# Performance work log

Measured on AMD Instinct MI355X. Metric: run time of the kernel, lower is better.

The kernel has to match this reference:

```python
import jax, jax.numpy as jnp
import numpy as np

N, E = 50000, 1600000
IN, OUT, H = 128, 32, 2
NT, ET = 20, 4
ETE, EAE, ED = 16, 16, 16
SLOPE = 0.2  # conv_neg_slope


def setup_inputs() -> dict:
    key = jax.random.key(0)
    ks = jax.random.split(key, 11)
    d_att = 2 * OUT + ETE + EAE
    return dict(
        x=jax.random.normal(ks[0], (N, IN), jnp.float32),
        edge_index=jax.random.randint(ks[1], (2, E), 0, N),
        ntypes=jax.random.randint(ks[2], (N,), 0, NT),
        etypes=jax.random.randint(ks[3], (E,), 0, ET),
        eattr=jax.random.normal(ks[4], (E, ED), jnp.float32),
        het_W=jax.random.normal(ks[5], (NT, IN, OUT), jnp.float32) / np.sqrt(IN).astype(np.float32),
        het_b=jnp.zeros((NT, OUT), jnp.float32),
        etype_table=jax.random.normal(ks[6], (ET, ETE), jnp.float32),
        eattr_W=jax.random.normal(ks[7], (ED, EAE), jnp.float32) / np.sqrt(ED).astype(np.float32),
        att_W=jax.random.normal(ks[8], (d_att, H), jnp.float32) / np.sqrt(d_att).astype(np.float32),
        lin_W=jax.random.normal(ks[9], (OUT + EAE, OUT), jnp.float32) / np.sqrt(OUT + EAE).astype(np.float32),
    )


def _lrelu(v):
    return jax.nn.leaky_relu(v, SLOPE)


def _heat_conv(x, edge_index, ntypes, etypes, eattr,
               het_W, het_b, etype_table, eattr_W, att_W, lin_W):
    # HeteroLinear: node-type-conditioned linear transform (loop over 20 types,
    # avoids materializing a [N, IN, OUT] gathered-weight tensor)
    h = jnp.zeros((x.shape[0], het_W.shape[-1]), x.dtype)
    for t in range(het_W.shape[0]):
        h = h + jnp.where((ntypes == t)[:, None], x @ het_W[t] + het_b[t], 0.0)

    src, dst = edge_index[0], edge_index[1]
    ete = _lrelu(etype_table[etypes])        # [E, ETE] edge-type embedding
    ea = _lrelu(eattr @ eattr_W)             # [E, EAE] edge-attr embedding
    x_i = h[dst]                             # target node feats [E, OUT]
    x_j = h[src]                             # source node feats [E, OUT]

    feat = jnp.concatenate([x_i, x_j, ete, ea], axis=-1)
    alpha = _lrelu(feat @ att_W)             # [E, H] raw attention logits

    # softmax grouped by destination node, per head
    amax = jax.ops.segment_max(alpha, dst, num_segments=N)  # [N, H]
    alpha = jnp.exp(alpha - amax[dst])
    denom = jax.ops.segment_sum(alpha, dst, num_segments=N)  # [N, H]
    alpha = alpha / denom[dst]

    msg = jnp.concatenate([x_j, ea], axis=-1) @ lin_W        # [E, OUT]
    m = (msg[:, None, :] * alpha[:, :, None]).reshape(alpha.shape[0], H * OUT)
    out = jax.ops.segment_sum(m, dst, num_segments=N)        # [N, H*OUT]
    return out  # concat=True -> flattened heads


def reference(x, edge_index, ntypes, etypes, eattr,
              het_W, het_b, etype_table, eattr_W, att_W, lin_W):
    out = _heat_conv(x, edge_index, ntypes, etypes, eattr,
                     het_W, het_b, etype_table, eattr_W, att_W, lin_W)
    return jax.nn.relu(out)  # final activation in forward (eval mode: no dropout)
```

## Files before the change

kernel.cpp:

```cpp
#include <hip/hip_runtime.h>
#include <hip/hip_fp16.h>

#define NN 50000
#define EE 1600000
#define IN_F 128
#define OUT_F 32
#define NHEAD 2
#define ETE_F 16
#define EAE_F 16
#define ED_F 16
#define D_ATT 96
#define SLOPE 0.2f
#define NB_SCAN 196

__global__ __launch_bounds__(256) void k_hetlin(
    const float* __restrict__ x, const int* __restrict__ ntypes,
    const float* __restrict__ hetW, const float* __restrict__ hetb,
    float* __restrict__ h)
{
    int tid = blockIdx.x * 256 + threadIdx.x;
    int n = tid >> 5;
    int o = tid & 31;
    if (n >= NN) return;
    int t = ntypes[n];
    const float* W = hetW + (size_t)t * IN_F * OUT_F + o;
    const float* xr = x + (size_t)n * IN_F;
    float acc = hetb[t * OUT_F + o];
    #pragma unroll 8
    for (int k = 0; k < IN_F; ++k)
        acc += xr[k] * W[(size_t)k * OUT_F];
    h[(size_t)n * OUT_F + o] = acc;
}

__global__ __launch_bounds__(256) void k_count(
    const int* __restrict__ dst, int* __restrict__ count)
{
    int e = blockIdx.x * 256 + threadIdx.x;
    atomicAdd(&count[dst[e]], 1);
}

__global__ __launch_bounds__(256) void k_scanA(
    const int* __restrict__ count, int* __restrict__ offsets,
    int* __restrict__ bsum)
{
    __shared__ int s[256];
    int t = threadIdx.x;
    int i = blockIdx.x * 256 + t;
    int c = (i < NN) ? count[i] : 0;
    s[t] = c;
    __syncthreads();
    for (int off = 1; off < 256; off <<= 1) {
        int v = (t >= off) ? s[t - off] : 0;
        __syncthreads();
        s[t] += v;
        __syncthreads();
    }
    if (i < NN) offsets[i] = s[t] - c;
    if (t == 255) bsum[blockIdx.x] = s[255];
}

__global__ __launch_bounds__(256) void k_scanB(
    const int* __restrict__ bsum, int* __restrict__ bbase)
{
    __shared__ int s[256];
    int t = threadIdx.x;
    int c = (t < NB_SCAN) ? bsum[t] : 0;
    s[t] = c;
    __syncthreads();
    for (int off = 1; off < 256; off <<= 1) {
        int v = (t >= off) ? s[t - off] : 0;
        __syncthreads();
        s[t] += v;
        __syncthreads();
    }
    if (t < NB_SCAN) bbase[t] = s[t] - c;
}

__global__ __launch_bounds__(256) void k_scanC(
    int* __restrict__ offsets, const int* __restrict__ bbase,
    int* __restrict__ next)
{
    int t = threadIdx.x;
    int i = blockIdx.x * 256 + t;
    if (i < NN) {
        int v = offsets[i] + bbase[blockIdx.x];
        offsets[i] = v;
        next[i] = v;
    }
    if (i == 0) offsets[NN] = EE;
}

__global__ __launch_bounds__(256) void k_edge2(
    const int* __restrict__ src, const int* __restrict__ dst,
    const int* __restrict__ etypes, const float* __restrict__ eattr,
    const float* __restrict__ etab, const float* __restrict__ eaW,
    const float* __restrict__ attW, const float* __restrict__ linW,
    const float* __restrict__ h, int* __restrict__ next,
    __half* __restrict__ msgbuf, __half2* __restrict__ expbuf)
{
    __shared__ float sEaW[ED_F * EAE_F];
    __shared__ float sAtt[D_ATT * NHEAD];
    __shared__ float sLin[48 * OUT_F];
    __shared__ float sEte[4 * ETE_F];

    int tid = threadIdx.x;
    for (int i = tid; i < ED_F * EAE_F; i += 256) sEaW[i] = eaW[i];
    for (int i = tid; i < D_ATT * NHEAD; i += 256) sAtt[i] = attW[i];
    for (int i = tid; i < 48 * OUT_F; i += 256) sLin[i] = linW[i];
    for (int i = tid; i < 4 * ETE_F; i += 256) {
        float v = etab[i];
        sEte[i] = v > 0.0f ? v : SLOPE * v;
    }
    __syncthreads();

    int e = blockIdx.x * 256 + tid;
    int s = src[e], d = dst[e], et = etypes[e];
    int slot = atomicAdd(&next[d], 1);

    float attr[ED_F];
    {
        const float4* ap = (const float4*)(eattr + (size_t)e * ED_F);
        #pragma unroll
        for (int q = 0; q < 4; ++q) {
            float4 v = ap[q];
            attr[4*q+0] = v.x; attr[4*q+1] = v.y;
            attr[4*q+2] = v.z; attr[4*q+3] = v.w;
        }
    }
    float ea[EAE_F];
    #pragma unroll
    for (int j = 0; j < EAE_F; ++j) {
        float acc = 0.0f;
        #pragma unroll
        for (int k = 0; k < ED_F; ++k) acc += attr[k] * sEaW[k * EAE_F + j];
        ea[j] = acc > 0.0f ? acc : SLOPE * acc;
    }

    float al0 = 0.0f, al1 = 0.0f;
    {
        const float4* hp = (const float4*)(h + (size_t)d * OUT_F);
        #pragma unroll
        for (int q = 0; q < 8; ++q) {
            float4 v = hp[q];
            al0 += v.x * sAtt[(4*q+0)*2] + v.y * sAtt[(4*q+1)*2]
                 + v.z * sAtt[(4*q+2)*2] + v.w * sAtt[(4*q+3)*2];
            al1 += v.x * sAtt[(4*q+0)*2+1] + v.y * sAtt[(4*q+1)*2+1]
                 + v.z * sAtt[(4*q+2)*2+1] + v.w * sAtt[(4*q+3)*2+1];
        }
    }
    float hs[OUT_F];
    {
        const float4* hp = (const float4*)(h + (size_t)s * OUT_F);
        #pragma unroll
        for (int q = 0; q < 8; ++q) {
            float4 v = hp[q];
            hs[4*q+0] = v.x; hs[4*q+1] = v.y; hs[4*q+2] = v.z; hs[4*q+3] = v.w;
        }
        #pragma unroll
        for (int k = 0; k < OUT_F; ++k) {
            al0 += hs[k] * sAtt[(OUT_F + k) * 2];
            al1 += hs[k] * sAtt[(OUT_F + k) * 2 + 1];
        }
    }
    #pragma unroll
    for (int k = 0; k < ETE_F; ++k) {
        float v = sEte[et * ETE_F + k];
        al0 += v * sAtt[(64 + k) * 2];
        al1 += v * sAtt[(64 + k) * 2 + 1];
    }
    #pragma unroll
    for (int k = 0; k < EAE_F; ++k) {
        al0 += ea[k] * sAtt[(80 + k) * 2];
        al1 += ea[k] * sAtt[(80 + k) * 2 + 1];
    }
    al0 = al0 > 0.0f ? al0 : SLOPE * al0;
    al1 = al1 > 0.0f ? al1 : SLOPE * al1;
    float e0 = __expf(al0), e1 = __expf(al1);

    float msg[OUT_F];
    #pragma unroll
    for (int o = 0; o < OUT_F; ++o) {
        float acc = 0.0f;
        #pragma unroll
        for (int k = 0; k < OUT_F; ++k) acc += hs[k] * sLin[k * OUT_F + o];
        #pragma unroll
        for (int k = 0; k < EAE_F; ++k) acc += ea[k] * sLin[(OUT_F + k) * OUT_F + o];
        msg[o] = acc;
    }

    expbuf[slot] = __floats2half2_rn(e0, e1);
    __half2 mh[16];
    #pragma unroll
    for (int q = 0; q < 16; ++q) mh[q] = __floats2half2_rn(msg[2*q], msg[2*q+1]);
    float4* mp = (float4*)(msgbuf + (size_t)slot * 32);
    const float4* s4 = (const float4*)mh;
    #pragma unroll
    for (int q = 0; q < 4; ++q) mp[q] = s4[q];
}

__global__ __launch_bounds__(256) void k_gather(
    const int* __restrict__ offsets, const __half* __restrict__ msgbuf,
    const __half2* __restrict__ expbuf, float* __restrict__ out)
{
    int tid = blockIdx.x * 256 + threadIdx.x;
    int n = tid >> 6;
    int lane = tid & 63;
    if (n >= NN) return;
    int o = lane & 31, hh = lane >> 5;
    int s0 = offsets[n], s1 = offsets[n + 1];

    float accm = 0.0f, accp = 0.0f;
    int slot = s0;
    for (; slot + 1 < s1; slot += 2) {
        float m0 = __half2float(msgbuf[(size_t)slot * 32 + o]);
        __half2 ev0 = expbuf[slot];
        float m1 = __half2float(msgbuf[(size_t)(slot + 1) * 32 + o]);
        __half2 ev1 = expbuf[slot + 1];
        float p0 = hh ? __high2float(ev0) : __low2float(ev0);
        float p1 = hh ? __high2float(ev1) : __low2float(ev1);
        accm += m0 * p0;
        accm += m1 * p1;
        accp += p0 + p1;
    }
    if (slot < s1) {
        float m0 = __half2float(msgbuf[(size_t)slot * 32 + o]);
        __half2 ev0 = expbuf[slot];
        float p0 = hh ? __high2float(ev0) : __low2float(ev0);
        accm += m0 * p0;
        accp += p0;
    }
    float v = accp > 0.0f ? accm / accp : 0.0f;
    out[(size_t)n * 64 + lane] = v > 0.0f ? v : 0.0f;
}

extern "C" void kernel_launch(void* const* d_in, const int* in_sizes, int n_in,
                              void* d_out, int out_size, void* d_ws, size_t ws_size,
                              hipStream_t stream)
{
    const float* x      = (const float*)d_in[0];
    const int*   eidx   = (const int*)  d_in[1];
    const int*   ntypes = (const int*)  d_in[2];
    const int*   etypes = (const int*)  d_in[3];
    const float* eattr  = (const float*)d_in[4];
    const float* hetW   = (const float*)d_in[5];
    const float* hetb   = (const float*)d_in[6];
    const float* etab   = (const float*)d_in[7];
    const float* eaW    = (const float*)d_in[8];
    const float* attW   = (const float*)d_in[9];
    const float* linW   = (const float*)d_in[10];
    float* out = (float*)d_out;

    char* ws = (char*)d_ws;
    size_t off = 0;
    auto alloc = [&](size_t bytes) {
        char* p = ws + off;
        off = (off + bytes + 255) & ~(size_t)255;
        return p;
    };
    float*   h       = (float*)  alloc((size_t)NN * 32 * sizeof(float));
    int*     count   = (int*)    alloc((size_t)NN * sizeof(int));
    int*     offsets = (int*)    alloc(((size_t)NN + 1) * sizeof(int));
    int*     next    = (int*)    alloc((size_t)NN * sizeof(int));
    int*     bsum    = (int*)    alloc(256 * sizeof(int));
    int*     bbase   = (int*)    alloc(256 * sizeof(int));
    __half2* expbuf  = (__half2*)alloc((size_t)EE * sizeof(__half2));
    __half*  msgbuf  = (__half*) alloc((size_t)EE * 32 * sizeof(__half));
    (void)ws_size;

    const int* srcp = eidx;
    const int* dstp = eidx + EE;

    hipMemsetAsync(count, 0, (size_t)NN * sizeof(int), stream);

    k_hetlin<<<(NN * 32 + 255) / 256, 256, 0, stream>>>(x, ntypes, hetW, hetb, h);
    k_count<<<EE / 256, 256, 0, stream>>>(dstp, count);
    k_scanA<<<NB_SCAN, 256, 0, stream>>>(count, offsets, bsum);
    k_scanB<<<1, 256, 0, stream>>>(bsum, bbase);
    k_scanC<<<NB_SCAN, 256, 0, stream>>>(offsets, bbase, next);
    k_edge2<<<EE / 256, 256, 0, stream>>>(srcp, dstp, etypes, eattr,
                                          etab, eaW, attW, linW, h, next,
                                          msgbuf, expbuf);
    k_gather<<<(NN * 64 + 255) / 256, 256, 0, stream>>>(offsets, msgbuf, expbuf, out);
}
```

Before: 564.3 us.

## Precompute per-node linear and attention terms, fuse edge compute with segmented reduction

The per-edge 32x32 message matmul and the node attention dot products are moved to a per-node k_post kernel, since they depend only on h, so each edge just gathers hlin[src] and scalar attention parts. The edge-type attention term is folded into an 8-value table. Edges are processed in dst-sorted order through an eid list, and each block reduces contiguous dst segments in shared memory. Segments fully inside a block are written directly, while boundary segments use atomics and a final normalisation kernel. This removes the fp16 message and exp buffers and the separate gather pass, at the cost of scattered eattr reads through the permutation and an extra fill kernel.

Result: slower. 608.9 us (+7.9%).

```diff
diff --git a/kernel.cpp b/kernel.cpp
--- a/kernel.cpp
+++ b/kernel.cpp
@@ -1,15 +1,9 @@
 #include <hip/hip_runtime.h>
-#include <hip/hip_fp16.h>
 
 #define NN 50000
 #define EE 1600000
 #define IN_F 128
 #define OUT_F 32
-#define NHEAD 2
-#define ETE_F 16
-#define EAE_F 16
-#define ED_F 16
-#define D_ATT 96
 #define SLOPE 0.2f
 #define NB_SCAN 196
 
@@ -32,6 +26,41 @@
     h[(size_t)n * OUT_F + o] = acc;
 }
 
+__global__ __launch_bounds__(256) void k_post(
+    const float* __restrict__ h, const float* __restrict__ linW,
+    const float* __restrict__ attW, float* __restrict__ hlin,
+    float* __restrict__ auxS, float* __restrict__ auxD)
+{
+    __shared__ float sH[8 * 33];
+    __shared__ float sLin[32 * 32];
+    int tid = threadIdx.x;
+    for (int i = tid; i < 1024; i += 256) sLin[i] = linW[i];
+    int g = tid >> 5, o = tid & 31;
+    int n = blockIdx.x * 8 + g;
+    float hv = h[(size_t)n * 32 + o];
+    sH[g * 33 + o] = hv;
+    __syncthreads();
+
+    float acc = 0.0f;
+    #pragma unroll
+    for (int k = 0; k < 32; ++k) acc += sH[g * 33 + k] * sLin[k * 32 + o];
+    hlin[(size_t)n * 32 + o] = acc;
+
+    float p0 = hv * attW[o * 2],        p1 = hv * attW[o * 2 + 1];
+    float p2 = hv * attW[(32 + o) * 2], p3 = hv * attW[(32 + o) * 2 + 1];
+    #pragma unroll
+    for (int m = 16; m >= 1; m >>= 1) {
+        p0 += __shfl_xor(p0, m, 32);
+        p1 += __shfl_xor(p1, m, 32);
+        p2 += __shfl_xor(p2, m, 32);
+        p3 += __shfl_xor(p3, m, 32);
+    }
+    if (o == 0) {
+        auxD[n * 2] = p0; auxD[n * 2 + 1] = p1;
+        auxS[n * 2] = p2; auxS[n * 2 + 1] = p3;
+    }
+}
+
 __global__ __launch_bounds__(256) void k_count(
     const int* __restrict__ dst, int* __restrict__ count)
 {
@@ -60,10 +89,22 @@
 }
 
 __global__ __launch_bounds__(256) void k_scanB(
-    const int* __restrict__ bsum, int* __restrict__ bbase)
+    const int* __restrict__ bsum, int* __restrict__ bbase,
+    const float* __restrict__ etab, const float* __restrict__ attW,
+    float* __restrict__ etedot)
 {
     __shared__ int s[256];
     int t = threadIdx.x;
+    if (t < 8) {
+        int et = t >> 1, hh = t & 1;
+        float acc = 0.0f;
+        for (int k = 0; k < 16; ++k) {
+            float v = etab[et * 16 + k];
+            v = v > 0.0f ? v : SLOPE * v;
+            acc += v * attW[(64 + k) * 2 + hh];
+        }
+        etedot[t] = acc;
+    }
     int c = (t < NB_SCAN) ? bsum[t] : 0;
     s[t] = c;
     __syncthreads();
@@ -90,36 +131,44 @@
     if (i == 0) offsets[NN] = EE;
 }
 
-__global__ __launch_bounds__(256) void k_edge2(
-    const int* __restrict__ src, const int* __restrict__ dst,
+__global__ __launch_bounds__(256) void k_fill(
+    const int* __restrict__ dst, int* __restrict__ next,
+    int* __restrict__ eidlist)
+{
+    int e = blockIdx.x * 256 + threadIdx.x;
+    int slot = atomicAdd(&next[dst[e]], 1);
+    eidlist[slot] = e;
+}
+
+__global__ __launch_bounds__(256) void k_main(
+    const int* __restrict__ eidlist, const int* __restrict__ offsets,
+    const int* __restrict__ srcp, const int* __restrict__ dstp,
     const int* __restrict__ etypes, const float* __restrict__ eattr,
-    const float* __restrict__ etab, const float* __restrict__ eaW,
-    const float* __restrict__ attW, const float* __restrict__ linW,
-    const float* __restrict__ h, int* __restrict__ next,
-    __half* __restrict__ msgbuf, __half2* __restrict__ expbuf)
-{
-    __shared__ float sEaW[ED_F * EAE_F];
-    __shared__ float sAtt[D_ATT * NHEAD];
-    __shared__ float sLin[48 * OUT_F];
-    __shared__ float sEte[4 * ETE_F];
+    const float* __restrict__ eaW, const float* __restrict__ attW,
+    const float* __restrict__ linW, const float* __restrict__ etedot,
+    const float* __restrict__ hlin, const float* __restrict__ auxS,
+    const float* __restrict__ auxD,
+    float* __restrict__ out, float* __restrict__ numbuf,
+    float* __restrict__ denombuf)
+{
+    __shared__ float sMsg[256 * 33];
+    __shared__ float sP[256 * 2];
+    __shared__ int   sDst[256];
+    __shared__ int   sWCnt[4];
+    __shared__ int   sSegStart[256];
+    __shared__ int   sSegNode[256];
 
     int tid = threadIdx.x;
-    for (int i = tid; i < ED_F * EAE_F; i += 256) sEaW[i] = eaW[i];
-    for (int i = tid; i < D_ATT * NHEAD; i += 256) sAtt[i] = attW[i];
-    for (int i = tid; i < 48 * OUT_F; i += 256) sLin[i] = linW[i];
-    for (int i = tid; i < 4 * ETE_F; i += 256) {
-        float v = etab[i];
-        sEte[i] = v > 0.0f ? v : SLOPE * v;
-    }
-    __syncthreads();
-
-    int e = blockIdx.x * 256 + tid;
-    int s = src[e], d = dst[e], et = etypes[e];
-    int slot = atomicAdd(&next[d], 1);
-
-    float attr[ED_F];
+    int s = blockIdx.x * 256 + tid;
+    int eid = eidlist[s];
+    int src = srcp[eid];
+    int d   = dstp[eid];
+    int et  = etypes[eid];
+    sDst[tid] = d;
+
+    float attr[16];
     {
-        const float4* ap = (const float4*)(eattr + (size_t)e * ED_F);
+        const float4* ap = (const float4*)(eattr + (size_t)eid * 16);
         #pragma unroll
         for (int q = 0; q < 4; ++q) {
             float4 v = ap[q];
@@ -127,110 +176,111 @@
             attr[4*q+2] = v.z; attr[4*q+3] = v.w;
         }
     }
-    float ea[EAE_F];
-    #pragma unroll
-    for (int j = 0; j < EAE_F; ++j) {
+    float ea[16];
+    #pragma unroll
+    for (int j = 0; j < 16; ++j) {
         float acc = 0.0f;
         #pragma unroll
-        for (int k = 0; k < ED_F; ++k) acc += attr[k] * sEaW[k * EAE_F + j];
+        for (int k = 0; k < 16; ++k) acc += attr[k] * eaW[k * 16 + j];
         ea[j] = acc > 0.0f ? acc : SLOPE * acc;
     }
 
-    float al0 = 0.0f, al1 = 0.0f;
+    float2 aD = ((const float2*)auxD)[d];
+    float2 aS = ((const float2*)auxS)[src];
+    float2 eD = ((const float2*)etedot)[et];
+    float al0 = aD.x + aS.x + eD.x;
+    float al1 = aD.y + aS.y + eD.y;
+    #pragma unroll
+    for (int j = 0; j < 16; ++j) {
+        al0 += ea[j] * attW[(80 + j) * 2];
+        al1 += ea[j] * attW[(80 + j) * 2 + 1];
+    }
+    al0 = al0 > 0.0f ? al0 : SLOPE * al0;
+    al1 = al1 > 0.0f ? al1 : SLOPE * al1;
+    float p0 = __expf(al0), p1 = __expf(al1);
+
+    float msg[32];
     {
-        const float4* hp = (const float4*)(h + (size_t)d * OUT_F);
+        const float4* hp = (const float4*)(hlin + (size_t)src * 32);
         #pragma unroll
         for (int q = 0; q < 8; ++q) {
             float4 v = hp[q];
-            al0 += v.x * sAtt[(4*q+0)*2] + v.y * sAtt[(4*q+1)*2]
-                 + v.z * sAtt[(4*q+2)*2] + v.w * sAtt[(4*q+3)*2];
-            al1 += v.x * sAtt[(4*q+0)*2+1] + v.y * sAtt[(4*q+1)*2+1]
-                 + v.z * sAtt[(4*q+2)*2+1] + v.w * sAtt[(4*q+3)*2+1];
-        }
-    }
-    float hs[OUT_F];
-    {
-        const float4* hp = (const float4*)(h + (size_t)s * OUT_F);
+            msg[4*q+0] = v.x; msg[4*q+1] = v.y;
+            msg[4*q+2] = v.z; msg[4*q+3] = v.w;
+        }
+    }
+    #pragma unroll
+    for (int j = 0; j < 16; ++j) {
+        float e = ea[j];
         #pragma unroll
-        for (int q = 0; q < 8; ++q) {
-            float4 v = hp[q];
-            hs[4*q+0] = v.x; hs[4*q+1] = v.y; hs[4*q+2] = v.z; hs[4*q+3] = v.w;
-        }
-        #pragma unroll
-        for (int k = 0; k < OUT_F; ++k) {
-            al0 += hs[k] * sAtt[(OUT_F + k) * 2];
-            al1 += hs[k] * sAtt[(OUT_F + k) * 2 + 1];
-        }
-    }
-    #pragma unroll
-    for (int k = 0; k < ETE_F; ++k) {
-        float v = sEte[et * ETE_F + k];
-        al0 += v * sAtt[(64 + k) * 2];
-        al1 += v * sAtt[(64 + k) * 2 + 1];
-    }
-    #pragma unroll
-    for (int k = 0; k < EAE_F; ++k) {
-        al0 += ea[k] * sAtt[(80 + k) * 2];
-        al1 += ea[k] * sAtt[(80 + k) * 2 + 1];
-    }
-    al0 = al0 > 0.0f ? al0 : SLOPE * al0;
-    al1 = al1 > 0.0f ? al1 : SLOPE * al1;
-    float e0 = __expf(al0), e1 = __expf(al1);
-
-    float msg[OUT_F];
-    #pragma unroll
-    for (int o = 0; o < OUT_F; ++o) {
-        float acc = 0.0f;
-        #pragma unroll
-        for (int k = 0; k < OUT_F; ++k) acc += hs[k] * sLin[k * OUT_F + o];
-        #pragma unroll
-        for (int k = 0; k < EAE_F; ++k) acc += ea[k] * sLin[(OUT_F + k) * OUT_F + o];
-        msg[o] = acc;
-    }
-
-    expbuf[slot] = __floats2half2_rn(e0, e1);
-    __half2 mh[16];
-    #pragma unroll
-    for (int q = 0; q < 16; ++q) mh[q] = __floats2half2_rn(msg[2*q], msg[2*q+1]);
-    float4* mp = (float4*)(msgbuf + (size_t)slot * 32);
-    const float4* s4 = (const float4*)mh;
-    #pragma unroll
-    for (int q = 0; q < 4; ++q) mp[q] = s4[q];
-}
-
-__global__ __launch_bounds__(256) void k_gather(
-    const int* __restrict__ offsets, const __half* __restrict__ msgbuf,
-    const __half2* __restrict__ expbuf, float* __restrict__ out)
-{
-    int tid = blockIdx.x * 256 + threadIdx.x;
-    int n = tid >> 6;
-    int lane = tid & 63;
-    if (n >= NN) return;
-    int o = lane & 31, hh = lane >> 5;
-    int s0 = offsets[n], s1 = offsets[n + 1];
-
-    float accm = 0.0f, accp = 0.0f;
-    int slot = s0;
-    for (; slot + 1 < s1; slot += 2) {
-        float m0 = __half2float(msgbuf[(size_t)slot * 32 + o]);
-        __half2 ev0 = expbuf[slot];
-        float m1 = __half2float(msgbuf[(size_t)(slot + 1) * 32 + o]);
-        __half2 ev1 = expbuf[slot + 1];
-        float p0 = hh ? __high2float(ev0) : __low2float(ev0);
-        float p1 = hh ? __high2float(ev1) : __low2float(ev1);
-        accm += m0 * p0;
-        accm += m1 * p1;
-        accp += p0 + p1;
-    }
-    if (slot < s1) {
-        float m0 = __half2float(msgbuf[(size_t)slot * 32 + o]);
-        __half2 ev0 = expbuf[slot];
-        float p0 = hh ? __high2float(ev0) : __low2float(ev0);
-        accm += m0 * p0;
-        accp += p0;
-    }
-    float v = accp > 0.0f ? accm / accp : 0.0f;
-    out[(size_t)n * 64 + lane] = v > 0.0f ? v : 0.0f;
+        for (int o = 0; o < 32; ++o) msg[o] += e * linW[(32 + j) * 32 + o];
+    }
+
+    #pragma unroll
+    for (int o = 0; o < 32; ++o) sMsg[tid * 33 + o] = msg[o];
+    sP[tid * 2 + 0] = p0;
+    sP[tid * 2 + 1] = p1;
+    __syncthreads();
+
+    int ln = tid & 63, wv = tid >> 6;
+    bool isStart = (tid == 0) || (sDst[tid - 1] != d);
+    unsigned long long bm = __ballot(isStart);
+    int wrank = __popcll(bm & ((1ull << ln) - 1ull));
+    if (ln == 0) sWCnt[wv] = __popcll(bm);
+    __syncthreads();
+    int base = 0, nSeg = 0;
+    #pragma unroll
+    for (int w = 0; w < 4; ++w) {
+        int c = sWCnt[w];
+        if (w < wv) base += c;
+        nSeg += c;
+    }
+    if (isStart) {
+        int sid = base + wrank;
+        sSegStart[sid] = tid;
+        sSegNode[sid] = d;
+    }
+    __syncthreads();
+
+    int o = ln & 31, hh = ln >> 5;
+    int gs = blockIdx.x * 256;
+    for (int g = wv; g < nSeg; g += 4) {
+        int a = sSegStart[g];
+        int b = (g + 1 < nSeg) ? sSegStart[g + 1] : 256;
+        int n = sSegNode[g];
+        float accm = 0.0f, accp = 0.0f;
+        for (int tt = a; tt < b; ++tt) {
+            float p = sP[tt * 2 + hh];
+            accm += p * sMsg[tt * 33 + o];
+            accp += p;
+        }
+        int o0 = offsets[n], o1 = offsets[n + 1];
+        bool interior = (o0 == gs + a) && (o1 == gs + b);
+        if (interior) {
+            float v = accm / accp;
+            out[(size_t)n * 64 + ln] = v > 0.0f ? v : 0.0f;
+            if (o == 0) denombuf[n * 2 + hh] = -1.0f;
+        } else {
+            atomicAdd(&numbuf[(size_t)n * 64 + ln], accm);
+            if (o == 0) atomicAdd(&denombuf[n * 2 + hh], accp);
+        }
+    }
+}
+
+__global__ __launch_bounds__(256) void k_final(
+    float* __restrict__ out, const float* __restrict__ numbuf,
+    const float* __restrict__ denombuf)
+{
+    int i = blockIdx.x * 256 + threadIdx.x;
+    int n = i >> 6;
+    int hh = (i >> 5) & 1;
+    float dn = denombuf[n * 2 + hh];
+    if (dn > 0.0f) {
+        float v = numbuf[i] / dn;
+        out[i] = v > 0.0f ? v : 0.0f;
+    } else if (dn == 0.0f) {
+        out[i] = 0.0f;
+    }
 }
 
 extern "C" void kernel_launch(void* const* d_in, const int* in_sizes, int n_in,
@@ -257,28 +307,37 @@
         off = (off + bytes + 255) & ~(size_t)255;
         return p;
     };
-    float*   h       = (float*)  alloc((size_t)NN * 32 * sizeof(float));
-    int*     count   = (int*)    alloc((size_t)NN * sizeof(int));
-    int*     offsets = (int*)    alloc(((size_t)NN + 1) * sizeof(int));
-    int*     next    = (int*)    alloc((size_t)NN * sizeof(int));
-    int*     bsum    = (int*)    alloc(256 * sizeof(int));
-    int*     bbase   = (int*)    alloc(256 * sizeof(int));
-    __half2* expbuf  = (__half2*)alloc((size_t)EE * sizeof(__half2));
-    __half*  msgbuf  = (__half*) alloc((size_t)EE * 32 * sizeof(__half));
+    float* h        = (float*)alloc((size_t)NN * 32 * sizeof(float));
+    float* hlin     = (float*)alloc((size_t)NN * 32 * sizeof(float));
+    float* auxS     = (float*)alloc((size_t)NN * 2 * sizeof(float));
+    float* auxD     = (float*)alloc((size_t)NN * 2 * sizeof(float));
+    float* etedot   = (float*)alloc(8 * sizeof(float));
+    int*   count    = (int*)  alloc((size_t)NN * sizeof(int));
+    int*   offsets  = (int*)  alloc(((size_t)NN + 1) * sizeof(int));
+    int*   next     = (int*)  alloc((size_t)NN * sizeof(int));
+    int*   bsum     = (int*)  alloc(256 * sizeof(int));
+    int*   bbase    = (int*)  alloc(256 * sizeof(int));
+    int*   eidlist  = (int*)  alloc((size_t)EE * sizeof(int));
+    float* numbuf   = (float*)alloc((size_t)NN * 64 * sizeof(float));
+    float* denombuf = (float*)alloc((size_t)NN * 2 * sizeof(float));
     (void)ws_size;
 
     const int* srcp = eidx;
     const int* dstp = eidx + EE;
 
-    hipMemsetAsync(count, 0, (size_t)NN * sizeof(int), stream);
-
-    k_hetlin<<<(NN * 32 + 255) / 256, 256, 0, stream>>>(x, ntypes, hetW, hetb, h);
+    hipMemsetAsync(count,    0, (size_t)NN * sizeof(int), stream);
+    hipMemsetAsync(numbuf,   0, (size_t)NN * 64 * sizeof(float), stream);
+    hipMemsetAsync(denombuf, 0, (size_t)NN * 2 * sizeof(float), stream);
+
+    k_hetlin<<<(NN * 32) / 256, 256, 0, stream>>>(x, ntypes, hetW, hetb, h);
+    k_post<<<NN / 8, 256, 0, stream>>>(h, linW, attW, hlin, auxS, auxD);
     k_count<<<EE / 256, 256, 0, stream>>>(dstp, count);
     k_scanA<<<NB_SCAN, 256, 0, stream>>>(count, offsets, bsum);
-    k_scanB<<<1, 256, 0, stream>>>(bsum, bbase);
+    k_scanB<<<1, 256, 0, stream>>>(bsum, bbase, etab, attW, etedot);
     k_scanC<<<NB_SCAN, 256, 0, stream>>>(offsets, bbase, next);
-    k_edge2<<<EE / 256, 256, 0, stream>>>(srcp, dstp, etypes, eattr,
-                                          etab, eaW, attW, linW, h, next,
-                                          msgbuf, expbuf);
-    k_gather<<<(NN * 64 + 255) / 256, 256, 0, stream>>>(offsets, msgbuf, expbuf, out);
-}
+    k_fill<<<EE / 256, 256, 0, stream>>>(dstp, next, eidlist);
+    k_main<<<EE / 256, 256, 0, stream>>>(eidlist, offsets, srcp, dstp, etypes,
+                                         eattr, eaW, attW, linW, etedot,
+                                         hlin, auxS, auxD, out, numbuf, denombuf);
+    k_final<<<(NN * 64) / 256, 256, 0, stream>>>(out, numbuf, denombuf);
+}
```
